# Optimization experiments

Hardware: AMD Instinct MI355X
Metric: run time of the kernel (lower is better)

## Reference

```python
import jax, jax.numpy as jnp
import numpy as np
import math

B, N, D = 8, 4096, 768
H, M, L = 12, 64, 4
HD = D // H  # 64
TEMP = 1.0
EPS = 1e-5


def layer_norm(x, g, b):
    m = jnp.mean(x, axis=-1, keepdims=True)
    v = jnp.mean((x - m) ** 2, axis=-1, keepdims=True)
    return (x - m) * jax.lax.rsqrt(v + EPS) * g + b


def setup_inputs() -> dict:
    key = jax.random.key(0)
    ks = jax.random.split(key, 24)
    s = 0.02
    inp = {
        "latent_tokens": jax.random.normal(ks[0], (B, N, D), jnp.float32),
        "selector": jax.random.normal(ks[1], (M, D), jnp.float32) * s,
        "qc": jax.random.normal(ks[2], (L, M, D), jnp.float32) * s,
        "qw": jax.random.normal(ks[3], (L, H, D, HD), jnp.float32) * s,
        "qb": jnp.zeros((L, H, HD), jnp.float32),
        "kw": jax.random.normal(ks[4], (L, H, D, HD), jnp.float32) * s,
        "kb": jnp.zeros((L, H, HD), jnp.float32),
        "vw": jax.random.normal(ks[5], (L, H, D, HD), jnp.float32) * s,
        "vb": jnp.zeros((L, H, HD), jnp.float32),
        "hw": jax.random.normal(ks[6], (L, H, HD, HD), jnp.float32) * s,
        "hb": jnp.zeros((L, H, HD), jnp.float32),
        "ow": jax.random.normal(ks[7], (L, D, D), jnp.float32) * s,
        "ob": jnp.zeros((L, D), jnp.float32),
        "w1": jax.random.normal(ks[8], (L, D, 4 * D), jnp.float32) * s,
        "b1": jnp.zeros((L, 4 * D), jnp.float32),
        "w2": jax.random.normal(ks[9], (L, 4 * D, D), jnp.float32) * s,
        "b2": jnp.zeros((L, D), jnp.float32),
        "g1": jnp.ones((L, D), jnp.float32),
        "beta1": jnp.zeros((L, D), jnp.float32),
        "g2": jnp.ones((L, D), jnp.float32),
        "beta2": jnp.zeros((L, D), jnp.float32),
    }
    return inp


def reference(latent_tokens, selector, qc, qw, qb, kw, kb, vw, vb, hw, hb,
              ow, ob, w1, b1, w2, b2, g1, beta1, g2, beta2):
    scale = 1.0 / math.sqrt(HD)
    # soft-selection pooling of encoder tokens into M pos queries
    logits = jnp.einsum('bnd,md->bmn', latent_tokens, selector)
    weights = jax.nn.softmax(logits / TEMP, axis=-1)
    x = jnp.einsum('bmn,bnd->bmd', weights, latent_tokens)  # [B,M,D]
    for l in range(L):
        queries = qc[l][None] + x                                    # [B,M,D]
        q = jnp.einsum('bmd,hde->bhme', queries, qw[l]) + qb[l][None, :, None, :]
        k = jnp.einsum('bnd,hde->bhne', latent_tokens, kw[l]) + kb[l][None, :, None, :]
        v = jnp.einsum('bnd,hde->bhne', latent_tokens, vw[l]) + vb[l][None, :, None, :]
        attn = jax.nn.softmax(jnp.einsum('bhme,bhne->bhmn', q, k) * scale, axis=-1)
        o = jnp.einsum('bhmn,bhne->bhme', attn, v)                   # [B,H,M,HD]
        o = jnp.einsum('bhme,hef->bhmf', o, hw[l]) + hb[l][None, :, None, :]
        o = o.transpose(0, 2, 1, 3).reshape(o.shape[0], M, D)        # concat heads
        o = o @ ow[l] + ob[l]
        x1 = layer_norm(o + queries, g1[l], beta1[l])
        mlp = jax.nn.gelu(x1 @ w1[l] + b1[l], approximate=False) @ w2[l] + b2[l]
        x = layer_norm(x1 + mlp, g2[l], beta2[l])
    return x
```

## Files before the change

### kernel.cpp

```cpp
#include <hip/hip_runtime.h>
#include <hip/hip_bf16.h>


using bf16 = __hip_bfloat16;
typedef __attribute__((ext_vector_type(8))) __bf16 bf16x8;
typedef __attribute__((ext_vector_type(4))) float f32x4;
typedef unsigned int u32;
typedef __attribute__((ext_vector_type(4))) u32 u32x4;

#define DEVINL __device__ __forceinline__

DEVINL float bf2f(bf16 v) { return __bfloat162float(v); }
DEVINL bf16 f2bf(float v) { return __float2bfloat16(v); }
DEVINL u32 f2bfu(float f) { bf16 h = __float2bfloat16(f); return *(unsigned short*)&h; }
DEVINL float gelu_f(float x) { return 0.5f * x * (1.0f + erff(x * 0.70710678118654752f)); }

DEVINL void async16(const bf16* g, bf16* l) {
  __builtin_amdgcn_global_load_lds(
      (const __attribute__((address_space(1))) u32*)g,
      (__attribute__((address_space(3))) u32*)l, 16, 0, 0);
}

DEVINL u32 xcd_swizzle(u32 id, u32 nwg) {
  u32 q = nwg >> 3, r = nwg & 7;
  u32 xcd = id & 7, pos = id >> 3;
  return xcd * q + (xcd < r ? xcd : r) + pos;
}

__global__ __launch_bounds__(256) void cvt_f2b(const float* in, bf16* out, long n) {
  const long i = ((long)blockIdx.x * 256 + threadIdx.x) * 8;
  if (i >= n) return;
  float4 a = *(const float4*)(in + i);
  float4 b = *(const float4*)(in + i + 4);
  u32 w[4];
  w[0] = f2bfu(a.x) | (f2bfu(a.y) << 16);
  w[1] = f2bfu(a.z) | (f2bfu(a.w) << 16);
  w[2] = f2bfu(b.x) | (f2bfu(b.y) << 16);
  w[3] = f2bfu(b.z) | (f2bfu(b.w) << 16);
  *(u32x4*)(out + i) = *(u32x4*)w;
}

struct GemmKVP {
  const bf16* A;
  const bf16* Bk;
  const bf16* Bv;
  bf16* Ck;
  bf16* Cv;
  const float* biask;
  const float* biasv;
};

__global__ __launch_bounds__(256, 2) void gemm_kv(GemmKVP p) {
  __shared__ __align__(16) bf16 SH[36864];
  bf16* As = SH;
  bf16* Ks = SH + 12288;
  bf16* Vs = SH + 24576;
  const int tid = threadIdx.x;
  const int wave = tid >> 6, lane = tid & 63;

  u32 id = blockIdx.x + 6u * blockIdx.y;
  id = xcd_swizzle(id, 1536);
  const int bn = id % 6;
  const int bm = id / 6;

  const bf16* Ag = p.A + (long)bm * 128 * 768;
  const bf16* Kg = p.Bk + (long)bn * 128 * 768;
  const bf16* Vg = p.Bv + (long)bn * 128 * 768;

  const int cq = (((tid & 3) ^ ((tid >> 3) & 3))) * 8;
  const long ro = (long)(tid >> 2) * 768 + cq;
  const long r1 = ro + (long)64 * 768;
  const bf16* ga0 = Ag + ro; const bf16* ga1 = Ag + r1;
  const bf16* gk0 = Kg + ro; const bf16* gk1 = Kg + r1;
  const bf16* gv0 = Vg + ro; const bf16* gv1 = Vg + r1;

  const int m_in = lane & 15, q = lane >> 4;
  const int wm = (wave & 1) * 64, wn = (wave >> 1) * 64;
  const int sw3 = (q ^ ((m_in >> 1) & 3)) << 3;
  f32x4 acck[4][4] = {};
  f32x4 accv[4][4] = {};
  const int nk = 24;

  auto stage = [&](int s, int ko) {
    async16(ga0 + ko, As + s * 4096 + tid * 8);
    async16(ga1 + ko, As + s * 4096 + 2048 + tid * 8);
    async16(gk0 + ko, Ks + s * 4096 + tid * 8);
    async16(gk1 + ko, Ks + s * 4096 + 2048 + tid * 8);
    async16(gv0 + ko, Vs + s * 4096 + tid * 8);
    async16(gv1 + ko, Vs + s * 4096 + 2048 + tid * 8);
  };
  stage(0, 0);
  stage(1, 32);

  int slot = 0;
  for (int k = 0; k < nk; ++k) {
    if (k + 1 < nk) asm volatile("s_waitcnt vmcnt(6)" ::: "memory");
    else            asm volatile("s_waitcnt vmcnt(0)" ::: "memory");
    __builtin_amdgcn_s_barrier();
    if (k + 2 < nk) {
      int ns = slot + 2; if (ns >= 3) ns -= 3;
      stage(ns, (k + 2) * 32);
    }
    const bf16* Ac = As + slot * 4096;
    const bf16* Kc = Ks + slot * 4096;
    const bf16* Vc = Vs + slot * 4096;
    bf16x8 af[4], bfr[4];
#pragma unroll
    for (int i = 0; i < 4; i++)
      af[i] = *(const bf16x8*)(Ac + (wm + i * 16 + m_in) * 32 + sw3);
#pragma unroll
    for (int j = 0; j < 4; j++)
      bfr[j] = *(const bf16x8*)(Kc + (wn + j * 16 + m_in) * 32 + sw3);
#pragma unroll
    for (int i = 0; i < 4; i++)
#pragma unroll
      for (int j = 0; j < 4; j++)
        acck[i][j] = __builtin_amdgcn_mfma_f32_16x16x32_bf16(af[i], bfr[j], acck[i][j], 0, 0, 0);
#pragma unroll
    for (int j = 0; j < 4; j++)
      bfr[j] = *(const bf16x8*)(Vc + (wn + j * 16 + m_in) * 32 + sw3);
#pragma unroll
    for (int i = 0; i < 4; i++)
#pragma unroll
      for (int j = 0; j < 4; j++)
        accv[i][j] = __builtin_amdgcn_mfma_f32_16x16x32_bf16(af[i], bfr[j], accv[i][j], 0, 0, 0);
    slot = (slot + 1 == 3) ? 0 : slot + 1;
  }

  const long row0 = (long)bm * 128 + wm + q * 4;
  const long col0 = (long)bn * 128 + wn + m_in;
  const int bb = (bm * 128) >> 12;
  const int nn0 = (bm * 128) & 4095;
#pragma unroll
  for (int i = 0; i < 4; i++)
#pragma unroll
    for (int j = 0; j < 4; j++) {
      long r = row0 + i * 16;
      long c = col0 + j * 16;
      float bk_ = p.biask[c];
#pragma unroll
      for (int t = 0; t < 4; t++)
        p.Ck[(r + t) * 768 + c] = f2bf(acck[i][j][t] + bk_);
    }
  __syncthreads();
  bf16* VT = SH;
#pragma unroll
  for (int i = 0; i < 4; i++) {
    const int nb = wm + q * 4 + i * 16;
    const int sl = nb >> 3;
    const int of = nb & 7;
#pragma unroll
    for (int j = 0; j < 4; j++) {
      const int e = wn + j * 16 + m_in;
      const float bv_ = p.biasv[bn * 128 + e];
      u32 w0 = f2bfu(accv[i][j][0] + bv_) | (f2bfu(accv[i][j][1] + bv_) << 16);
      u32 w1 = f2bfu(accv[i][j][2] + bv_) | (f2bfu(accv[i][j][3] + bv_) << 16);
      uint2 pk; pk.x = w0; pk.y = w1;
      *(uint2*)(VT + e * 128 + ((sl ^ (e & 15)) << 3) + of) = pk;
    }
  }
  __syncthreads();
  bf16* CvB = p.Cv + (long)bb * 3145728;
#pragma unroll
  for (int k2 = 0; k2 < 8; k2++) {
    int g = tid + k2 * 256;
    int e = g >> 4, sc = g & 15;
    u32x4 vv = *(const u32x4*)(VT + e * 128 + ((sc ^ (e & 15)) << 3));
    *(u32x4*)(CvB + (long)(bn * 128 + e) * 4096 + nn0 + sc * 8) = vv;
  }
}

struct GemmSmP {
  const bf16* A; const bf16* B; void* C; const float* bias; const float* res;
  long sA1, sA2, sB1, sB2, sC1, sC2, sBias2;
  int nb2, lda, ldb, ldc, K;
  int bias_mode;
  int out_mode;
  float scale;
};

__global__ __launch_bounds__(256, 4) void gemm_sm(GemmSmP p) {
  __shared__ __align__(16) bf16 As[3][64 * 32];
  __shared__ __align__(16) bf16 Bs[3][64 * 32];
  const int tid = threadIdx.x;
  const int wave = tid >> 6, lane = tid & 63;

  const u32 gx = gridDim.x, gy = gridDim.y;
  u32 id = blockIdx.x + gx * (blockIdx.y + gy * blockIdx.z);
  id = xcd_swizzle(id, gx * gy * gridDim.z);
  const int bn = id % gx;
  const u32 t2 = id / gx;
  const int bm = t2 % gy;
  const int bz = t2 / gy;

  const int z1 = bz / p.nb2, z2 = bz - z1 * p.nb2;
  const bf16* Ag = p.A + p.sA1 * z1 + p.sA2 * z2 + (long)bm * 64 * p.lda;
  const bf16* Bg = p.B + p.sB1 * z1 + p.sB2 * z2 + (long)bn * 64 * p.ldb;

  const int cq = (((tid & 3) ^ ((tid >> 3) & 3))) * 8;
  const bf16* gpa = Ag + ((long)(tid >> 2) * p.lda + cq);
  const bf16* gpb = Bg + ((long)(tid >> 2) * p.ldb + cq);

  const int m_in = lane & 15, q = lane >> 4;
  const int wm = (wave & 1) * 32, wn = (wave >> 1) * 32;
  const int sw3 = (q ^ ((m_in >> 1) & 3)) << 3;
  f32x4 acc[2][2] = {};
  const int nk = p.K >> 5;

  async16(gpa, &As[0][0] + tid * 8);
  async16(gpb, &Bs[0][0] + tid * 8);
  if (nk > 1) {
    async16(gpa + 32, &As[1][0] + tid * 8);
    async16(gpb + 32, &Bs[1][0] + tid * 8);
  }

  int slot = 0;
  for (int k = 0; k < nk; ++k) {
    if (k + 1 < nk) asm volatile("s_waitcnt vmcnt(2)" ::: "memory");
    else            asm volatile("s_waitcnt vmcnt(0)" ::: "memory");
    __builtin_amdgcn_s_barrier();
    if (k + 2 < nk) {
      int ns = slot + 2; if (ns >= 3) ns -= 3;
      const int ko = (k + 2) * 32;
      async16(gpa + ko, &As[ns][0] + tid * 8);
      async16(gpb + ko, &Bs[ns][0] + tid * 8);
    }
    const bf16* Ac = &As[slot][0];
    const bf16* Bc = &Bs[slot][0];
    bf16x8 a0 = *(const bf16x8*)(Ac + (wm + m_in) * 32 + sw3);
    bf16x8 a1 = *(const bf16x8*)(Ac + (wm + 16 + m_in) * 32 + sw3);
    bf16x8 b0 = *(const bf16x8*)(Bc + (wn + m_in) * 32 + sw3);
    bf16x8 b1 = *(const bf16x8*)(Bc + (wn + 16 + m_in) * 32 + sw3);
    acc[0][0] = __builtin_amdgcn_mfma_f32_16x16x32_bf16(a0, b0, acc[0][0], 0, 0, 0);
    acc[0][1] = __builtin_amdgcn_mfma_f32_16x16x32_bf16(a0, b1, acc[0][1], 0, 0, 0);
    acc[1][0] = __builtin_amdgcn_mfma_f32_16x16x32_bf16(a1, b0, acc[1][0], 0, 0, 0);
    acc[1][1] = __builtin_amdgcn_mfma_f32_16x16x32_bf16(a1, b1, acc[1][1], 0, 0, 0);
    slot = (slot + 1 == 3) ? 0 : slot + 1;
  }

  const long row0 = (long)bm * 64 + wm + q * 4;
  const long col0 = (long)bn * 64 + wn + m_in;
  const float* bias = p.bias + p.sBias2 * z2;
#pragma unroll
  for (int i = 0; i < 2; i++)
#pragma unroll
    for (int j = 0; j < 2; j++) {
      long r = row0 + i * 16;
      long cc = col0 + j * 16;
      float badd = (p.bias_mode == 1) ? bias[cc] : 0.f;
#pragma unroll
      for (int t = 0; t < 4; t++) {
        float v = acc[i][j][t] * p.scale + badd;
        long idx = (r + t) * p.ldc + cc;
        if (p.out_mode == 0) {
          float* Cf = (float*)p.C + p.sC1 * z1 + p.sC2 * z2;
          if (p.res) v += p.res[idx];
          Cf[idx] = v;
        } else {
          bf16* Cb = (bf16*)p.C + p.sC1 * z1 + p.sC2 * z2;
          if (p.out_mode == 2) v = gelu_f(v);
          Cb[idx] = f2bf(v);
        }
      }
    }
}

struct AttnP {
  const bf16* Q;
  const bf16* K;
  const bf16* VT;
  float* Opart;
  float* ML;
};

__global__ __launch_bounds__(256, 3) void attn_part(AttnP p) {
  __shared__ __align__(16) bf16 SH[24576];
  bf16* Qs = SH;
  bf16* Ks = SH + 4096;
  bf16* Vs = SH + 12288;
  bf16* Ps = SH + 20480;
  const int tid = threadIdx.x;
  const int wave = tid >> 6, lane = tid & 63;
  const int z = blockIdx.x, c = blockIdx.y;
  const int b = z / 12, h = z - b * 12;
  const int n0 = c * 512;

  const int sl0 = tid, sl1 = tid + 256;
  const int r0 = sl0 >> 3, r1 = sl1 >> 3;
  const int q0 = (sl0 & 7) ^ (r0 & 7), q1 = (sl1 & 7) ^ (r1 & 7);

  const bf16* Qg = p.Q + ((long)b * 64) * 768 + h * 64;
  const bf16* Kg = p.K + ((long)b * 4096 + n0) * 768 + h * 64;
  const bf16* Vg = p.VT + (long)b * 3145728 + (long)(h * 64) * 4096 + n0;

  async16(Qg + (long)r0 * 768 + q0 * 8, Qs + sl0 * 8);
  async16(Qg + (long)r1 * 768 + q1 * 8, Qs + sl1 * 8);
  auto stageK = [&](int s) {
    bf16* d = Ks + (s & 1) * 4096;
    async16(Kg + (long)(s * 64 + r0) * 768 + q0 * 8, d + sl0 * 8);
    async16(Kg + (long)(s * 64 + r1) * 768 + q1 * 8, d + sl1 * 8);
  };
  auto stageV = [&](int s) {
    bf16* d = Vs + (s & 1) * 4096;
    async16(Vg + (long)r0 * 4096 + s * 64 + q0 * 8, d + sl0 * 8);
    async16(Vg + (long)r1 * 4096 + s * 64 + q1 * 8, d + sl1 * 8);
  };
  stageK(0); stageV(0); stageK(1); stageV(1);

  const int m_in = lane & 15, q = lane >> 4;
  const int wm = wave * 16;

  asm volatile("s_waitcnt vmcnt(8)" ::: "memory");
  __builtin_amdgcn_s_barrier();

  bf16x8 qa[2];
  {
    const int ra = wm + m_in;
#pragma unroll
    for (int kk = 0; kk < 2; kk++)
      qa[kk] = *(const bf16x8*)(Qs + ra * 64 + ((((kk * 4 + q) ^ (ra & 7))) << 3));
  }

  f32x4 accO[4] = {};
  float m_run[4] = {-1e30f, -1e30f, -1e30f, -1e30f};
  float l_run[4] = {0.f, 0.f, 0.f, 0.f};

  for (int s = 0; s < 8; ++s) {
    if (s < 7) asm volatile("s_waitcnt vmcnt(4)" ::: "memory");
    else       asm volatile("s_waitcnt vmcnt(0)" ::: "memory");
    __builtin_amdgcn_s_barrier();
    const bf16* Kc = Ks + (s & 1) * 4096;
    const bf16* Vc = Vs + (s & 1) * 4096;
    f32x4 accS[4] = {};
#pragma unroll
    for (int kk = 0; kk < 2; kk++) {
#pragma unroll
      for (int j = 0; j < 4; j++) {
        const int rj = j * 16 + m_in;
        bf16x8 kb = *(const bf16x8*)(Kc + rj * 64 + ((((kk * 4 + q) ^ (rj & 7))) << 3));
        accS[j] = __builtin_amdgcn_mfma_f32_16x16x32_bf16(qa[kk], kb, accS[j], 0, 0, 0);
      }
    }
    float pe[4][4], osc[4];
#pragma unroll
    for (int t = 0; t < 4; t++) {
      float mx = fmaxf(fmaxf(accS[0][t], accS[1][t]), fmaxf(accS[2][t], accS[3][t])) * 0.125f;
      mx = fmaxf(mx, __shfl_xor(mx, 1));
      mx = fmaxf(mx, __shfl_xor(mx, 2));
      mx = fmaxf(mx, __shfl_xor(mx, 4));
      mx = fmaxf(mx, __shfl_xor(mx, 8));
      const float mnew = fmaxf(m_run[t], mx);
      const float so = __expf(m_run[t] - mnew);
      float rs = 0.f;
#pragma unroll
      for (int j = 0; j < 4; j++) {
        float e = __expf(accS[j][t] * 0.125f - mnew);
        pe[j][t] = e; rs += e;
      }
      rs += __shfl_xor(rs, 1); rs += __shfl_xor(rs, 2);
      rs += __shfl_xor(rs, 4); rs += __shfl_xor(rs, 8);
      l_run[t] = l_run[t] * so + rs;
      m_run[t] = mnew;
      osc[t] = so;
    }
#pragma unroll
    for (int ef = 0; ef < 4; ef++)
#pragma unroll
      for (int t = 0; t < 4; t++) accO[ef][t] *= osc[t];
#pragma unroll
    for (int j = 0; j < 4; j++) {
      const int pc = m_in + 16 * j;
#pragma unroll
      for (int t = 0; t < 4; t++) {
        const int pm = wm + q * 4 + t;
        Ps[pm * 64 + (((pc >> 3) ^ (pm & 7)) << 3) + (pc & 7)] = f2bf(pe[j][t]);
      }
    }
    const int ra = wm + m_in;
#pragma unroll
    for (int kk = 0; kk < 2; kk++) {
      bf16x8 pa = *(const bf16x8*)(Ps + ra * 64 + ((((kk * 4 + q) ^ (ra & 7))) << 3));
#pragma unroll
      for (int ef = 0; ef < 4; ef++) {
        const int rv = ef * 16 + m_in;
        bf16x8 vb = *(const bf16x8*)(Vc + rv * 64 + ((((kk * 4 + q) ^ (rv & 7))) << 3));
        accO[ef] = __builtin_amdgcn_mfma_f32_16x16x32_bf16(pa, vb, accO[ef], 0, 0, 0);
      }
    }
    __builtin_amdgcn_s_barrier();
    if (s < 6) { stageK(s + 2); stageV(s + 2); }
  }

  float* Og = p.Opart + ((long)c * 96 + z) * 4096;
#pragma unroll
  for (int ef = 0; ef < 4; ef++)
#pragma unroll
    for (int t = 0; t < 4; t++)
      Og[(wm + q * 4 + t) * 64 + ef * 16 + m_in] = accO[ef][t];
  if (m_in == 0) {
    float* ml = p.ML + ((long)c * 96 + z) * 128;
#pragma unroll
    for (int t = 0; t < 4; t++) {
      ml[wm + q * 4 + t] = m_run[t];
      ml[64 + wm + q * 4 + t] = l_run[t];
    }
  }
}

struct AttnC { const float* Opart; const float* ML; bf16* O; };

__global__ __launch_bounds__(256) void attn_comb(AttnC p) {
  const int tid = threadIdx.x;
  const int gidx = blockIdx.x * 4 + (tid >> 6);
  const int lane = tid & 63;
  const int z = gidx >> 6, m = gidx & 63;
  float mv[8];
  float mx = -1e30f;
#pragma unroll
  for (int c = 0; c < 8; c++) {
    mv[c] = p.ML[((long)c * 96 + z) * 128 + m];
    mx = fmaxf(mx, mv[c]);
  }
  float l = 0.f, o = 0.f;
#pragma unroll
  for (int c = 0; c < 8; c++) {
    const float w = __expf(mv[c] - mx);
    l += w * p.ML[((long)c * 96 + z) * 128 + 64 + m];
    o += w * p.Opart[(((long)c * 96 + z) * 64 + m) * 64 + lane];
  }
  p.O[((long)z * 64 + m) * 64 + lane] = f2bf(o / l);
}

struct TrP { const float* in; bf16* out; bf16* outR; int R, C; long sIn, sOut, sOutR; };

__global__ __launch_bounds__(256) void transpose_f2b(TrP p) {
  __shared__ __align__(16) bf16 tile[64][80];
  const int tid = threadIdx.x;
  const int ct = blockIdx.x, rt = blockIdx.y, z = blockIdx.z;
  const float* in = p.in + p.sIn * z + ((long)rt * 64) * p.C + (long)ct * 64;
  bf16* out = p.out + p.sOut * z + ((long)ct * 64) * p.R + (long)rt * 64;
  bf16* outR = p.outR ? p.outR + p.sOutR * z + ((long)rt * 64) * p.C + (long)ct * 64 : nullptr;
  const int r = tid >> 3, c8 = (tid & 7) * 8;
#pragma unroll
  for (int h = 0; h < 2; h++) {
    int rr = r + h * 32;
    float4 a = *(const float4*)(in + (long)rr * p.C + c8);
    float4 b = *(const float4*)(in + (long)rr * p.C + c8 + 4);
    u32 w[4];
    w[0] = f2bfu(a.x) | (f2bfu(a.y) << 16);
    w[1] = f2bfu(a.z) | (f2bfu(a.w) << 16);
    w[2] = f2bfu(b.x) | (f2bfu(b.y) << 16);
    w[3] = f2bfu(b.z) | (f2bfu(b.w) << 16);
    *(u32x4*)&tile[rr][c8] = *(u32x4*)w;
    if (outR) *(u32x4*)(outR + (long)rr * p.C + c8) = *(u32x4*)w;
  }
  __syncthreads();
  const int co = tid >> 3, r8 = (tid & 7) * 8;
#pragma unroll
  for (int h = 0; h < 2; h++) {
    int cc = co + h * 32;
    __align__(16) bf16 tmp[8];
#pragma unroll
    for (int j = 0; j < 8; j++) tmp[j] = tile[r8 + j][cc];
    *(u32x4*)(out + (long)cc * p.R + r8) = *(const u32x4*)tmp;
  }
}

__global__ __launch_bounds__(256) void softmax_rows(bf16* X) {
  const long row = blockIdx.x;
  u32* x = (u32*)(X + row * 4096);
  const int tid = threadIdx.x;
  const int lane = tid & 63, wave = tid >> 6;
  u32 d[8];
  *(u32x4*)&d[0] = ((const u32x4*)x)[tid * 2];
  *(u32x4*)&d[4] = ((const u32x4*)x)[tid * 2 + 1];
  float v[16];
#pragma unroll
  for (int j = 0; j < 8; j++) {
    v[2 * j] = __uint_as_float(d[j] << 16);
    v[2 * j + 1] = __uint_as_float(d[j] & 0xffff0000u);
  }
  float m = v[0];
#pragma unroll
  for (int i = 1; i < 16; i++) m = fmaxf(m, v[i]);
  for (int off = 32; off; off >>= 1) m = fmaxf(m, __shfl_xor(m, off));
  __shared__ float sm1[4], sm2[4];
  if (lane == 0) sm1[wave] = m;
  __syncthreads();
  m = fmaxf(fmaxf(sm1[0], sm1[1]), fmaxf(sm1[2], sm1[3]));
  float s = 0.f;
#pragma unroll
  for (int i = 0; i < 16; i++) { v[i] = __expf(v[i] - m); s += v[i]; }
  for (int off = 32; off; off >>= 1) s += __shfl_xor(s, off);
  if (lane == 0) sm2[wave] = s;
  __syncthreads();
  s = sm2[0] + sm2[1] + sm2[2] + sm2[3];
  const float inv = 1.f / s;
#pragma unroll
  for (int j = 0; j < 8; j++) {
    u32 lo = f2bfu(v[2 * j] * inv);
    u32 hi = f2bfu(v[2 * j + 1] * inv);
    d[j] = lo | (hi << 16);
  }
  ((u32x4*)x)[tid * 2] = *(u32x4*)&d[0];
  ((u32x4*)x)[tid * 2 + 1] = *(u32x4*)&d[4];
}

__global__ __launch_bounds__(256) void ln_rows(const float* in, const float* g, const float* b,
                                               float* outf, bf16* outb,
                                               const float* qc, float* qf, bf16* qb16) {
  const long row = blockIdx.x;
  const float* x = in + row * 768;
  const int tid = threadIdx.x;
  const int lane = tid & 63, wave = tid >> 6;
  float v0 = x[tid], v1 = x[tid + 256], v2 = x[tid + 512];
  float s = v0 + v1 + v2;
  float s2 = v0 * v0 + v1 * v1 + v2 * v2;
  for (int off = 32; off; off >>= 1) { s += __shfl_xor(s, off); s2 += __shfl_xor(s2, off); }
  __shared__ float sa[4], sb[4];
  if (lane == 0) { sa[wave] = s; sb[wave] = s2; }
  __syncthreads();
  s = sa[0] + sa[1] + sa[2] + sa[3];
  s2 = sb[0] + sb[1] + sb[2] + sb[3];
  const float mean = s * (1.f / 768.f);
  const float var = s2 * (1.f / 768.f) - mean * mean;
  const float rs = rsqrtf(var + 1e-5f);
  float o0 = (v0 - mean) * rs * g[tid] + b[tid];
  float o1 = (v1 - mean) * rs * g[tid + 256] + b[tid + 256];
  float o2 = (v2 - mean) * rs * g[tid + 512] + b[tid + 512];
  if (outf) { float* of = outf + row * 768; of[tid] = o0; of[tid + 256] = o1; of[tid + 512] = o2; }
  if (outb) { bf16* ob = outb + row * 768; ob[tid] = f2bf(o0); ob[tid + 256] = f2bf(o1); ob[tid + 512] = f2bf(o2); }
  if (qc) {
    const float* qr = qc + (row & 63) * 768;
    float u0 = o0 + qr[tid], u1 = o1 + qr[tid + 256], u2 = o2 + qr[tid + 512];
    float* pf = qf + row * 768;
    pf[tid] = u0; pf[tid + 256] = u1; pf[tid + 512] = u2;
    bf16* pb = qb16 + row * 768;
    pb[tid] = f2bf(u0); pb[tid + 256] = f2bf(u1); pb[tid + 512] = f2bf(u2);
  }
}

struct CombP { const float* in; int nch; const float* bias; const float* res;
               float* outf; bf16* outb; const float* qc; float* qf; bf16* qb16; };

__global__ __launch_bounds__(256) void combine(CombP p) {
  const long i = (long)blockIdx.x * 256 + threadIdx.x;
  float s = 0.f;
  for (int c = 0; c < p.nch; c++) s += p.in[(long)c * 393216 + i];
  if (p.bias) s += p.bias[i % 768];
  if (p.res) s += p.res[i];
  if (p.outf) p.outf[i] = s;
  if (p.outb) p.outb[i] = f2bf(s);
  if (p.qc) {
    float v = s + p.qc[i % 49152];
    p.qf[i] = v;
    p.qb16[i] = f2bf(v);
  }
}

extern "C" void kernel_launch(void* const* d_in, const int* in_sizes, int n_in,
                              void* d_out, int out_size, void* d_ws, size_t ws_size,
                              hipStream_t stream) {
  (void)in_sizes; (void)n_in; (void)out_size; (void)ws_size;
  const float* tokens   = (const float*)d_in[0];
  const float* selector = (const float*)d_in[1];
  const float* qc  = (const float*)d_in[2];
  const float* qw  = (const float*)d_in[3];
  const float* qb  = (const float*)d_in[4];
  const float* kw  = (const float*)d_in[5];
  const float* kb  = (const float*)d_in[6];
  const float* vw  = (const float*)d_in[7];
  const float* vb  = (const float*)d_in[8];
  const float* hw  = (const float*)d_in[9];
  const float* hb  = (const float*)d_in[10];
  const float* ow  = (const float*)d_in[11];
  const float* ob  = (const float*)d_in[12];
  const float* w1  = (const float*)d_in[13];
  const float* b1  = (const float*)d_in[14];
  const float* w2  = (const float*)d_in[15];
  const float* b2  = (const float*)d_in[16];
  const float* g1  = (const float*)d_in[17];
  const float* be1 = (const float*)d_in[18];
  const float* g2  = (const float*)d_in[19];
  const float* be2 = (const float*)d_in[20];
  float* out = (float*)d_out;

  char* ws = (char*)d_ws;
  size_t off = 0;
  auto alloc = [&](size_t bytes) { char* pp = ws + off; off += (bytes + 255) & ~(size_t)255; return pp; };
  bf16* TOKT  = (bf16*)alloc(50331648);
  bf16* TOKB  = (bf16*)alloc(50331648);
  bf16* KBUF  = (bf16*)alloc(50331648);
  bf16* VTB   = (bf16*)alloc(50331648);
  bf16* PLOG  = (bf16*)alloc(4194304);
  bf16* SELB  = (bf16*)alloc(98304);
  bf16* QWT   = (bf16*)alloc(4718592);
  bf16* KWT   = (bf16*)alloc(4718592);
  bf16* VWT   = (bf16*)alloc(4718592);
  bf16* HWT   = (bf16*)alloc(393216);
  bf16* OWT   = (bf16*)alloc(4718592);
  bf16* W1T   = (bf16*)alloc(18874368);
  bf16* W2T   = (bf16*)alloc(18874368);
  bf16* QBUF  = (bf16*)alloc(786432);
  bf16* OBUF  = (bf16*)alloc(786432);
  bf16* O2BUF = (bf16*)alloc(786432);
  float* QF   = (float*)alloc(1572864);
  bf16* QB16  = (bf16*)alloc(786432);
  float* T1   = (float*)alloc(1572864);
  float* X1F  = (float*)alloc(1572864);
  bf16* X1B   = (bf16*)alloc(786432);
  bf16* H1    = (bf16*)alloc(3145728);
  float* T2   = (float*)alloc(1572864);
  float* OPART = (float*)alloc(12582912);
  float* MLB  = (float*)alloc(393216);

  auto tr = [&](const float* in, bf16* o, bf16* oR, int R, int C, long s, long sR, int slabs) {
    TrP t{in, o, oR, R, C, s, s, sR};
    transpose_f2b<<<dim3(C / 64, R / 64, slabs), 256, 0, stream>>>(t);
  };
  tr(tokens, TOKT, TOKB, 4096, 768, 3145728, 3145728, 8);
  cvt_f2b<<<24, 256, 0, stream>>>(selector, SELB, 49152);
  tr(qw, QWT, nullptr, 768, 64, 49152, 0, 48);
  tr(kw, KWT, nullptr, 768, 64, 49152, 0, 48);
  tr(vw, VWT, nullptr, 768, 64, 49152, 0, 48);
  tr(hw, HWT, nullptr, 64, 64, 4096, 0, 48);
  tr(ow, OWT, nullptr, 768, 768, 589824, 0, 4);
  tr(w1, W1T, nullptr, 768, 3072, 2359296, 0, 4);
  tr(w2, W2T, nullptr, 3072, 768, 2359296, 0, 4);

  {
    GemmSmP p{}; p.A = SELB; p.B = TOKB; p.C = PLOG;
    p.sB1 = 3145728; p.sC1 = 262144; p.nb2 = 1;
    p.lda = 768; p.ldb = 768; p.ldc = 4096; p.K = 768;
    p.bias_mode = 0; p.out_mode = 1; p.scale = 1.0f;
    gemm_sm<<<dim3(64, 1, 8), 256, 0, stream>>>(p);
  }
  softmax_rows<<<512, 256, 0, stream>>>(PLOG);
  {
    GemmSmP p{}; p.A = PLOG; p.B = TOKT; p.C = OPART;
    p.sA1 = 512; p.sA2 = 262144; p.sB1 = 512; p.sB2 = 3145728;
    p.sC1 = 393216; p.sC2 = 49152; p.nb2 = 8;
    p.lda = 4096; p.ldb = 4096; p.ldc = 768; p.K = 512;
    p.bias_mode = 0; p.out_mode = 0; p.scale = 1.0f;
    gemm_sm<<<dim3(12, 1, 64), 256, 0, stream>>>(p);
  }
  {
    CombP c{}; c.in = OPART; c.nch = 8; c.qc = qc; c.qf = QF; c.qb16 = QB16;
    combine<<<1536, 256, 0, stream>>>(c);
  }

  for (int l = 0; l < 4; l++) {
    {
      GemmSmP p{}; p.A = QB16; p.B = QWT + l * 589824; p.C = QBUF; p.bias = qb + l * 768;
      p.nb2 = 1; p.lda = 768; p.ldb = 768; p.ldc = 768; p.K = 768;
      p.bias_mode = 1; p.out_mode = 1; p.scale = 1.0f;
      gemm_sm<<<dim3(12, 8, 1), 256, 0, stream>>>(p);
    }
    {
      GemmKVP p{TOKB, KWT + l * 589824, VWT + l * 589824, KBUF, VTB,
                kb + l * 768, vb + l * 768};
      gemm_kv<<<dim3(6, 256, 1), 256, 0, stream>>>(p);
    }
    {
      AttnP p{QBUF, KBUF, VTB, OPART, MLB};
      attn_part<<<dim3(96, 8, 1), 256, 0, stream>>>(p);
      AttnC c{OPART, MLB, OBUF};
      attn_comb<<<1536, 256, 0, stream>>>(c);
    }
    {
      GemmSmP p{}; p.A = OBUF; p.B = HWT + l * 49152; p.C = O2BUF; p.bias = hb + l * 768;
      p.sA1 = 49152; p.sA2 = 4096; p.sB1 = 0; p.sB2 = 4096; p.sC1 = 49152; p.sC2 = 64; p.sBias2 = 64;
      p.nb2 = 12; p.lda = 64; p.ldb = 64; p.ldc = 768; p.K = 64;
      p.bias_mode = 1; p.out_mode = 1; p.scale = 1.0f;
      gemm_sm<<<dim3(1, 1, 96), 256, 0, stream>>>(p);
    }
    {
      GemmSmP p{}; p.A = O2BUF; p.B = OWT + l * 589824; p.C = OPART;
      p.sA1 = 192; p.sB1 = 192; p.sC1 = 393216; p.nb2 = 1;
      p.lda = 768; p.ldb = 768; p.ldc = 768; p.K = 192;
      p.bias_mode = 0; p.out_mode = 0; p.scale = 1.0f;
      gemm_sm<<<dim3(12, 8, 4), 256, 0, stream>>>(p);
    }
    { CombP c{}; c.in = OPART; c.nch = 4; c.bias = ob + l * 768; c.res = QF; c.outf = T1;
      combine<<<1536, 256, 0, stream>>>(c); }
    ln_rows<<<512, 256, 0, stream>>>(T1, g1 + l * 768, be1 + l * 768, X1F, X1B, nullptr, nullptr, nullptr);
    {
      GemmSmP p{}; p.A = X1B; p.B = W1T + l * 2359296; p.C = H1; p.bias = b1 + l * 3072;
      p.nb2 = 1; p.lda = 768; p.ldb = 768; p.ldc = 3072; p.K = 768;
      p.bias_mode = 1; p.out_mode = 2; p.scale = 1.0f;
      gemm_sm<<<dim3(48, 8, 1), 256, 0, stream>>>(p);
    }
    {
      GemmSmP p{}; p.A = H1; p.B = W2T + l * 2359296; p.C = OPART;
      p.sA1 = 384; p.sB1 = 384; p.sC1 = 393216; p.nb2 = 1;
      p.lda = 3072; p.ldb = 3072; p.ldc = 768; p.K = 384;
      p.bias_mode = 0; p.out_mode = 0; p.scale = 1.0f;
      gemm_sm<<<dim3(12, 8, 8), 256, 0, stream>>>(p);
    }
    { CombP c{}; c.in = OPART; c.nch = 8; c.bias = b2 + l * 768; c.res = X1F; c.outf = T2;
      combine<<<1536, 256, 0, stream>>>(c); }
    ln_rows<<<512, 256, 0, stream>>>(T2, g2 + l * 768, be2 + l * 768,
                                     (l == 3) ? out : nullptr, nullptr,
                                     (l < 3) ? (qc + (l + 1) * 49152) : nullptr, QF, QB16);
  }
}
```

Baseline: 1.099 ms.

## Fuse attention combine with head matmul, fuse combine with layernorm, deepen A prefetch

Result: faster. 1.075 ms (-2.2%).

```diff
diff --git a/kernel.cpp b/kernel.cpp
--- a/kernel.cpp
+++ b/kernel.cpp
@@ -51,10 +51,10 @@
 };
 
 __global__ __launch_bounds__(256, 2) void gemm_kv(GemmKVP p) {
-  __shared__ __align__(16) bf16 SH[36864];
+  __shared__ __align__(16) bf16 SH[40960];
   bf16* As = SH;
-  bf16* Ks = SH + 12288;
-  bf16* Vs = SH + 24576;
+  bf16* Ks = SH + 16384;
+  bf16* Vs = SH + 28672;
   const int tid = threadIdx.x;
   const int wave = tid >> 6, lane = tid & 63;
 
@@ -81,29 +81,28 @@
   f32x4 accv[4][4] = {};
   const int nk = 24;
 
-  auto stage = [&](int s, int ko) {
+  auto stageA = [&](int s, int ko) {
     async16(ga0 + ko, As + s * 4096 + tid * 8);
     async16(ga1 + ko, As + s * 4096 + 2048 + tid * 8);
+  };
+  auto stageKV = [&](int s, int ko) {
     async16(gk0 + ko, Ks + s * 4096 + tid * 8);
     async16(gk1 + ko, Ks + s * 4096 + 2048 + tid * 8);
     async16(gv0 + ko, Vs + s * 4096 + tid * 8);
     async16(gv1 + ko, Vs + s * 4096 + 2048 + tid * 8);
   };
-  stage(0, 0);
-  stage(1, 32);
-
-  int slot = 0;
+  stageA(0, 0); stageA(1, 32); stageKV(0, 0); stageA(2, 64); stageKV(1, 32);
+
   for (int k = 0; k < nk; ++k) {
-    if (k + 1 < nk) asm volatile("s_waitcnt vmcnt(6)" ::: "memory");
-    else            asm volatile("s_waitcnt vmcnt(0)" ::: "memory");
+    if (k < nk - 2)       asm volatile("s_waitcnt vmcnt(6)" ::: "memory");
+    else if (k == nk - 2) asm volatile("s_waitcnt vmcnt(4)" ::: "memory");
+    else                  asm volatile("s_waitcnt vmcnt(0)" ::: "memory");
     __builtin_amdgcn_s_barrier();
-    if (k + 2 < nk) {
-      int ns = slot + 2; if (ns >= 3) ns -= 3;
-      stage(ns, (k + 2) * 32);
-    }
-    const bf16* Ac = As + slot * 4096;
-    const bf16* Kc = Ks + slot * 4096;
-    const bf16* Vc = Vs + slot * 4096;
+    if (k + 3 < nk) stageA((k + 3) & 3, (k + 3) * 32);
+    if (k + 2 < nk) stageKV((k + 2) % 3, (k + 2) * 32);
+    const bf16* Ac = As + (k & 3) * 4096;
+    const bf16* Kc = Ks + (k % 3) * 4096;
+    const bf16* Vc = Vs + (k % 3) * 4096;
     bf16x8 af[4], bfr[4];
 #pragma unroll
     for (int i = 0; i < 4; i++)
@@ -124,7 +123,6 @@
 #pragma unroll
       for (int j = 0; j < 4; j++)
         accv[i][j] = __builtin_amdgcn_mfma_f32_16x16x32_bf16(af[i], bfr[j], accv[i][j], 0, 0, 0);
-    slot = (slot + 1 == 3) ? 0 : slot + 1;
   }
 
   const long row0 = (long)bm * 128 + wm + q * 4;
@@ -407,13 +405,29 @@
   }
 }
 
-struct AttnC { const float* Opart; const float* ML; bf16* O; };
-
-__global__ __launch_bounds__(256) void attn_comb(AttnC p) {
+struct AttnHMP {
+  const float* Opart;
+  const float* ML;
+  const bf16* HWT;
+  const float* hb;
+  bf16* O2;
+};
+
+__global__ __launch_bounds__(256) void attn_hm(AttnHMP p) {
+  __shared__ __align__(16) bf16 Os[4096];
+  __shared__ __align__(16) bf16 Hs[4096];
   const int tid = threadIdx.x;
-  const int gidx = blockIdx.x * 4 + (tid >> 6);
-  const int lane = tid & 63;
-  const int z = gidx >> 6, m = gidx & 63;
+  const int z = blockIdx.x;
+  const int b = z / 12, h = z - b * 12;
+
+  const int sl0 = tid, sl1 = tid + 256;
+  const int r0 = sl0 >> 3, r1 = sl1 >> 3;
+  const int q0 = (sl0 & 7) ^ (r0 & 7), q1 = (sl1 & 7) ^ (r1 & 7);
+  const bf16* Hg = p.HWT + h * 4096;
+  async16(Hg + r0 * 64 + q0 * 8, Hs + sl0 * 8);
+  async16(Hg + r1 * 64 + q1 * 8, Hs + sl1 * 8);
+
+  const int m = tid >> 2, e0 = (tid & 3) * 16;
   float mv[8];
   float mx = -1e30f;
 #pragma unroll
@@ -421,14 +435,53 @@
     mv[c] = p.ML[((long)c * 96 + z) * 128 + m];
     mx = fmaxf(mx, mv[c]);
   }
-  float l = 0.f, o = 0.f;
+  float l = 0.f;
+  float o[16] = {};
 #pragma unroll
   for (int c = 0; c < 8; c++) {
     const float w = __expf(mv[c] - mx);
     l += w * p.ML[((long)c * 96 + z) * 128 + 64 + m];
-    o += w * p.Opart[(((long)c * 96 + z) * 64 + m) * 64 + lane];
-  }
-  p.O[((long)z * 64 + m) * 64 + lane] = f2bf(o / l);
+    const float* Og = p.Opart + (((long)c * 96 + z) * 64 + m) * 64 + e0;
+#pragma unroll
+    for (int e = 0; e < 16; e++) o[e] += w * Og[e];
+  }
+  const float inv = 1.f / l;
+#pragma unroll
+  for (int half = 0; half < 2; half++) {
+    u32 wbuf[4];
+#pragma unroll
+    for (int j = 0; j < 4; j++)
+      wbuf[j] = f2bfu(o[half * 8 + 2 * j] * inv) | (f2bfu(o[half * 8 + 2 * j + 1] * inv) << 16);
+    const int sl = (e0 >> 3) + half;
+    *(u32x4*)(Os + m * 64 + ((sl ^ (m & 7)) << 3)) = *(u32x4*)wbuf;
+  }
+  asm volatile("s_waitcnt vmcnt(0)" ::: "memory");
+  __syncthreads();
+
+  const int wave = tid >> 6, lane = tid & 63;
+  const int m_in = lane & 15, q = lane >> 4;
+  const int wm = wave * 16;
+  f32x4 acc[4] = {};
+#pragma unroll
+  for (int kk = 0; kk < 2; kk++) {
+    const int ra = wm + m_in;
+    bf16x8 a = *(const bf16x8*)(Os + ra * 64 + ((((kk * 4 + q) ^ (ra & 7))) << 3));
+#pragma unroll
+    for (int j = 0; j < 4; j++) {
+      const int rb = j * 16 + m_in;
+      bf16x8 bv = *(const bf16x8*)(Hs + rb * 64 + ((((kk * 4 + q) ^ (rb & 7))) << 3));
+      acc[j] = __builtin_amdgcn_mfma_f32_16x16x32_bf16(a, bv, acc[j], 0, 0, 0);
+    }
+  }
+  bf16* O2r = p.O2 + ((long)b * 64) * 768 + h * 64;
+#pragma unroll
+  for (int j = 0; j < 4; j++) {
+    const int e2 = j * 16 + m_in;
+    const float badd = p.hb[h * 64 + e2];
+#pragma unroll
+    for (int t = 0; t < 4; t++)
+      O2r[(wm + q * 4 + t) * 768 + e2] = f2bf(acc[j][t] + badd);
+  }
 }
 
 struct TrP { const float* in; bf16* out; bf16* outR; int R, C; long sIn, sOut, sOutR; };
@@ -540,6 +593,54 @@
   }
 }
 
+struct CombLnP {
+  const float* in; int nch; const float* bias; const float* res;
+  const float* g; const float* b;
+  float* outf; bf16* outb;
+  const float* qc; float* qf; bf16* qb16;
+};
+
+__global__ __launch_bounds__(256) void comb_ln(CombLnP p) {
+  const long row = blockIdx.x;
+  const long base = row * 768;
+  const int tid = threadIdx.x;
+  const int lane = tid & 63, wave = tid >> 6;
+  float v0 = 0.f, v1 = 0.f, v2 = 0.f;
+  for (int c = 0; c < p.nch; c++) {
+    const float* x = p.in + (long)c * 393216 + base;
+    v0 += x[tid]; v1 += x[tid + 256]; v2 += x[tid + 512];
+  }
+  v0 += p.bias[tid]; v1 += p.bias[tid + 256]; v2 += p.bias[tid + 512];
+  if (p.res) {
+    const float* r = p.res + base;
+    v0 += r[tid]; v1 += r[tid + 256]; v2 += r[tid + 512];
+  }
+  float s = v0 + v1 + v2;
+  float s2 = v0 * v0 + v1 * v1 + v2 * v2;
+  for (int off = 32; off; off >>= 1) { s += __shfl_xor(s, off); s2 += __shfl_xor(s2, off); }
+  __shared__ float sa[4], sb[4];
+  if (lane == 0) { sa[wave] = s; sb[wave] = s2; }
+  __syncthreads();
+  s = sa[0] + sa[1] + sa[2] + sa[3];
+  s2 = sb[0] + sb[1] + sb[2] + sb[3];
+  const float mean = s * (1.f / 768.f);
+  const float var = s2 * (1.f / 768.f) - mean * mean;
+  const float rs = rsqrtf(var + 1e-5f);
+  float o0 = (v0 - mean) * rs * p.g[tid] + p.b[tid];
+  float o1 = (v1 - mean) * rs * p.g[tid + 256] + p.b[tid + 256];
+  float o2 = (v2 - mean) * rs * p.g[tid + 512] + p.b[tid + 512];
+  if (p.outf) { float* of = p.outf + base; of[tid] = o0; of[tid + 256] = o1; of[tid + 512] = o2; }
+  if (p.outb) { bf16* ob = p.outb + base; ob[tid] = f2bf(o0); ob[tid + 256] = f2bf(o1); ob[tid + 512] = f2bf(o2); }
+  if (p.qc) {
+    const float* qr = p.qc + (row & 63) * 768;
+    float u0 = o0 + qr[tid], u1 = o1 + qr[tid + 256], u2 = o2 + qr[tid + 512];
+    float* pf = p.qf + base;
+    pf[tid] = u0; pf[tid + 256] = u1; pf[tid + 512] = u2;
+    bf16* pb = p.qb16 + base;
+    pb[tid] = f2bf(u0); pb[tid + 256] = f2bf(u1); pb[tid + 512] = f2bf(u2);
+  }
+}
+
 struct CombP { const float* in; int nch; const float* bias; const float* res;
                float* outf; bf16* outb; const float* qc; float* qf; bf16* qb16; };
 
@@ -602,15 +703,12 @@
   bf16* W1T   = (bf16*)alloc(18874368);
   bf16* W2T   = (bf16*)alloc(18874368);
   bf16* QBUF  = (bf16*)alloc(786432);
-  bf16* OBUF  = (bf16*)alloc(786432);
   bf16* O2BUF = (bf16*)alloc(786432);
   float* QF   = (float*)alloc(1572864);
   bf16* QB16  = (bf16*)alloc(786432);
-  float* T1   = (float*)alloc(1572864);
   float* X1F  = (float*)alloc(1572864);
   bf16* X1B   = (bf16*)alloc(786432);
   bf16* H1    = (bf16*)alloc(3145728);
-  float* T2   = (float*)alloc(1572864);
   float* OPART = (float*)alloc(12582912);
   float* MLB  = (float*)alloc(393216);
 
@@ -664,15 +762,10 @@
     {
       AttnP p{QBUF, KBUF, VTB, OPART, MLB};
       attn_part<<<dim3(96, 8, 1), 256, 0, stream>>>(p);
-      AttnC c{OPART, MLB, OBUF};
-      attn_comb<<<1536, 256, 0, stream>>>(c);
     }
     {
-      GemmSmP p{}; p.A = OBUF; p.B = HWT + l * 49152; p.C = O2BUF; p.bias = hb + l * 768;
-      p.sA1 = 49152; p.sA2 = 4096; p.sB1 = 0; p.sB2 = 4096; p.sC1 = 49152; p.sC2 = 64; p.sBias2 = 64;
-      p.nb2 = 12; p.lda = 64; p.ldb = 64; p.ldc = 768; p.K = 64;
-      p.bias_mode = 1; p.out_mode = 1; p.scale = 1.0f;
-      gemm_sm<<<dim3(1, 1, 96), 256, 0, stream>>>(p);
+      AttnHMP p{OPART, MLB, HWT + l * 49152, hb + l * 768, O2BUF};
+      attn_hm<<<96, 256, 0, stream>>>(p);
     }
     {
       GemmSmP p{}; p.A = O2BUF; p.B = OWT + l * 589824; p.C = OPART;
@@ -681,9 +774,11 @@
       p.bias_mode = 0; p.out_mode = 0; p.scale = 1.0f;
       gemm_sm<<<dim3(12, 8, 4), 256, 0, stream>>>(p);
     }
-    { CombP c{}; c.in = OPART; c.nch = 4; c.bias = ob + l * 768; c.res = QF; c.outf = T1;
-      combine<<<1536, 256, 0, stream>>>(c); }
-    ln_rows<<<512, 256, 0, stream>>>(T1, g1 + l * 768, be1 + l * 768, X1F, X1B, nullptr, nullptr, nullptr);
+    {
+      CombLnP c{}; c.in = OPART; c.nch = 4; c.bias = ob + l * 768; c.res = QF;
+      c.g = g1 + l * 768; c.b = be1 + l * 768; c.outf = X1F; c.outb = X1B;
+      comb_ln<<<512, 256, 0, stream>>>(c);
+    }
     {
       GemmSmP p{}; p.A = X1B; p.B = W1T + l * 2359296; p.C = H1; p.bias = b1 + l * 3072;
       p.nb2 = 1; p.lda = 768; p.ldb = 768; p.ldc = 3072; p.K = 768;
@@ -697,10 +792,13 @@
       p.bias_mode = 0; p.out_mode = 0; p.scale = 1.0f;
       gemm_sm<<<dim3(12, 8, 8), 256, 0, stream>>>(p);
     }
-    { CombP c{}; c.in = OPART; c.nch = 8; c.bias = b2 + l * 768; c.res = X1F; c.outf = T2;
-      combine<<<1536, 256, 0, stream>>>(c); }
-    ln_rows<<<512, 256, 0, stream>>>(T2, g2 + l * 768, be2 + l * 768,
-                                     (l == 3) ? out : nullptr, nullptr,
-                                     (l < 3) ? (qc + (l + 1) * 49152) : nullptr, QF, QB16);
-  }
-}
+    {
+      CombLnP c{}; c.in = OPART; c.nch = 8; c.bias = b2 + l * 768; c.res = X1F;
+      c.g = g2 + l * 768; c.b = be2 + l * 768;
+      c.outf = (l == 3) ? out : nullptr;
+      c.qc = (l < 3) ? (qc + (l + 1) * 49152) : nullptr;
+      c.qf = QF; c.qb16 = QB16;
+      comb_ln<<<512, 256, 0, stream>>>(c);
+    }
+  }
+}
```
